# Optimization experiments

Hardware: AMD Instinct MI355X
Metric: run time of the kernel (lower is better)

Reference implementation:

```python
import jax, jax.numpy as jnp
import numpy as np

N_EMBED = 1024
HEAD_COUNT = 16
HEAD_SIZE = 64  # HEAD_COUNT * HEAD_SIZE == N_EMBED
SEQ = 2048
BATCH = 2


def setup_inputs() -> dict:
    key = jax.random.key(0)
    k_ix, k_q, k_k, k_v, k_p, k_b = jax.random.split(key, 6)
    scale = 1.0 / np.sqrt(N_EMBED)
    inp = {
        "ix": jax.random.normal(k_ix, (BATCH, SEQ, N_EMBED), dtype=jnp.float32),
        # per-head projection weights, stored as x @ W form: [H, C, D]
        "Wq": jax.random.normal(k_q, (HEAD_COUNT, N_EMBED, HEAD_SIZE), dtype=jnp.float32) * scale,
        "Wk": jax.random.normal(k_k, (HEAD_COUNT, N_EMBED, HEAD_SIZE), dtype=jnp.float32) * scale,
        "Wv": jax.random.normal(k_v, (HEAD_COUNT, N_EMBED, HEAD_SIZE), dtype=jnp.float32) * scale,
        # output projection (Linear with bias): y = x @ Wp + bp
        "Wp": jax.random.normal(k_p, (N_EMBED, N_EMBED), dtype=jnp.float32) * scale,
        "bp": jax.random.normal(k_b, (N_EMBED,), dtype=jnp.float32) * scale,
    }
    return inp


def reference(ix, Wq, Wk, Wv, Wp, bp):
    B, T, C = ix.shape
    # per-head projections: [B, H, T, D]
    Q = jnp.einsum("btc,hcd->bhtd", ix, Wq)
    K = jnp.einsum("btc,hcd->bhtd", ix, Wk)
    V = jnp.einsum("btc,hcd->bhtd", ix, Wv)
    # NOTE: faithful to source -- scores are MULTIPLIED by sqrt(C) (C = n_embed)
    scores = jnp.einsum("bhtd,bhsd->bhts", Q, K) * (C ** 0.5)
    causal = jnp.tril(jnp.ones((T, T), dtype=bool))
    scores = jnp.where(causal, scores, -jnp.inf)
    wei = jax.nn.softmax(scores, axis=-1)
    out = jnp.einsum("bhts,bhsd->bhtd", wei, V)
    # concat heads (matches torch.cat over per-head outputs along last dim)
    out = out.transpose(0, 2, 1, 3).reshape(B, T, -1)
    return out @ Wp + bp
```

## Files before the change

kernel.cpp:

```cpp
#include <hip/hip_runtime.h>

#define BATCH 2
#define SEQL  2048
#define NEMB  1024
#define NH    16
#define HD    64
#define MROWS (BATCH*SEQL)

typedef short bf16x8 __attribute__((ext_vector_type(8)));
typedef float f32x16 __attribute__((ext_vector_type(16)));

__device__ __forceinline__ unsigned short f2bf(float x) {
    union { float f; unsigned u; } v; v.f = x;
    unsigned r = v.u + 0x7FFFu + ((v.u >> 16) & 1u);
    return (unsigned short)(r >> 16);
}
__device__ __forceinline__ void split_bf16(float x, unsigned short& hi, unsigned short& lo) {
    hi = f2bf(x);
    union { unsigned u; float f; } h; h.u = ((unsigned)hi) << 16;
    lo = f2bf(x - h.f);
}

__device__ __forceinline__ int slot16(int chunk, int lane) {
    return chunk * 66 + (lane & 31) + 33 * (lane >> 5);
}

__global__ __launch_bounds__(256) void split_convert_kernel(
    const float* __restrict__ src,
    unsigned short* __restrict__ dhi, unsigned short* __restrict__ dlo)
{
    int i = (blockIdx.x * 256 + threadIdx.x) * 4;
    float4 v = *(const float4*)(src + i);
    unsigned short h[4], l[4];
    split_bf16(v.x, h[0], l[0]); split_bf16(v.y, h[1], l[1]);
    split_bf16(v.z, h[2], l[2]); split_bf16(v.w, h[3], l[3]);
    uint2 ph, pl;
    ph.x = h[0] | ((unsigned)h[1] << 16); ph.y = h[2] | ((unsigned)h[3] << 16);
    pl.x = l[0] | ((unsigned)l[1] << 16); pl.y = l[2] | ((unsigned)l[3] << 16);
    *(uint2*)(dhi + i) = ph;
    *(uint2*)(dlo + i) = pl;
}

__global__ __launch_bounds__(256) void transpose_convert_kernel(
    const float* __restrict__ Wq, const float* __restrict__ Wk,
    const float* __restrict__ Wv, const float* __restrict__ Wp,
    unsigned short* __restrict__ qhi, unsigned short* __restrict__ qlo,
    unsigned short* __restrict__ khi, unsigned short* __restrict__ klo,
    unsigned short* __restrict__ vhi, unsigned short* __restrict__ pt)
{
    __shared__ float tile[64][68];
    const int z = blockIdx.z, hb = blockIdx.y, c0 = blockIdx.x * 64;
    const float* src; int rstride; unsigned short* dhi; unsigned short* dlo;
    if (z == 0)      { src = Wq + (size_t)hb * 65536; rstride = 64;   dhi = qhi; dlo = qlo; }
    else if (z == 1) { src = Wk + (size_t)hb * 65536; rstride = 64;   dhi = khi; dlo = klo; }
    else if (z == 2) { src = Wv + (size_t)hb * 65536; rstride = 64;   dhi = vhi; dlo = nullptr; }
    else             { src = Wp + (size_t)hb * 64;    rstride = 1024; dhi = pt;  dlo = nullptr; }
    const int tid = threadIdx.x;
    #pragma unroll
    for (int i = 0; i < 4; ++i) {
        int fidx = i * 256 + tid;
        int r  = fidx >> 4;
        int dq = (fidx & 15) * 4;
        float4 v = *(const float4*)(src + (size_t)(c0 + r) * rstride + dq);
        *(float4*)&tile[r][dq] = v;
    }
    __syncthreads();
    #pragma unroll
    for (int i = 0; i < 4; ++i) {
        int fidx = i * 256 + tid;
        int d  = fidx >> 4;
        int cq = (fidx & 15) * 4;
        size_t base = (size_t)(hb * 64 + d) * 1024 + c0 + cq;
        unsigned short hh[4], ll[4];
        #pragma unroll
        for (int j = 0; j < 4; ++j) split_bf16(tile[cq + j][d], hh[j], ll[j]);
        uint2 ph; ph.x = hh[0] | ((unsigned)hh[1] << 16); ph.y = hh[2] | ((unsigned)hh[3] << 16);
        *(uint2*)(dhi + base) = ph;
        if (dlo) {
            uint2 pl; pl.x = ll[0] | ((unsigned)ll[1] << 16); pl.y = ll[2] | ((unsigned)ll[3] << 16);
            *(uint2*)(dlo + base) = pl;
        }
    }
}

__global__ __launch_bounds__(256, 2) void qkv_gemm(
    const unsigned short* __restrict__ Ahi, const unsigned short* __restrict__ Alo,
    const unsigned short* __restrict__ Bq_hi, const unsigned short* __restrict__ Bq_lo,
    const unsigned short* __restrict__ Bk_hi, const unsigned short* __restrict__ Bk_lo,
    const unsigned short* __restrict__ Bv_hi,
    unsigned short* __restrict__ Qhi, unsigned short* __restrict__ Qlo,
    unsigned short* __restrict__ Khi, unsigned short* __restrict__ Klo,
    unsigned short* __restrict__ Vt)
{
    __shared__ unsigned short smem[2][4][4224];

    const int z = blockIdx.z;
    const bool split = (z < 2);
    const unsigned short* __restrict__ Bhi = (z == 0) ? Bq_hi : (z == 1) ? Bk_hi : Bv_hi;
    const unsigned short* __restrict__ Blo = (z == 0) ? Bq_lo : Bk_lo;
    unsigned short* __restrict__ Ohi = (z == 0) ? Qhi : Khi;
    unsigned short* __restrict__ Olo = (z == 0) ? Qlo : Klo;
    const float oscale = (z == 0) ? 32.0f : 1.0f;

    const int m0 = blockIdx.x * 128;
    const int n0 = blockIdx.y * 128;
    const int tid  = threadIdx.x;
    const int wid  = tid >> 6, lane = tid & 63;
    const int wr   = wid >> 1, wc = wid & 1;

    int roff_[2], slot_[2];
    #pragma unroll
    for (int q = 0; q < 2; ++q) {
        int f   = q * 256 + tid;
        int row = f >> 2;
        int k8  = (f & 3) * 8;
        roff_[q] = row * 1024 + k8;
        slot_[q] = slot16((row >> 5) * 2 + (k8 >> 4), (row & 31) + 32 * ((k8 >> 3) & 1)) * 8;
    }
    const unsigned short* __restrict__ Ah = Ahi + (size_t)m0 * 1024;
    const unsigned short* __restrict__ Bh = Bhi + (size_t)n0 * 1024;
    const unsigned short* __restrict__ Al = split ? Alo + (size_t)m0 * 1024 : Ahi;
    const unsigned short* __restrict__ Bl = split ? Blo + (size_t)n0 * 1024 : Bhi;

    bf16x8 pah[2], pbh[2], pal[2], pbl[2];

    #define LOADT(KK)  do { _Pragma("unroll")                                   \
        for (int q = 0; q < 2; ++q) {                                           \
            pah[q] = *(const bf16x8*)(Ah + roff_[q] + (KK));                    \
            pbh[q] = *(const bf16x8*)(Bh + roff_[q] + (KK));                    \
            if (split) {                                                        \
                pal[q] = *(const bf16x8*)(Al + roff_[q] + (KK));                \
                pbl[q] = *(const bf16x8*)(Bl + roff_[q] + (KK));                \
            }                                                                   \
        } } while (0)

    #define WRITET(NB) do { _Pragma("unroll")                                   \
        for (int q = 0; q < 2; ++q) {                                           \
            *(bf16x8*)(&smem[NB][0][slot_[q]]) = pah[q];                        \
            *(bf16x8*)(&smem[NB][1][slot_[q]]) = pbh[q];                        \
            if (split) {                                                        \
                *(bf16x8*)(&smem[NB][2][slot_[q]]) = pal[q];                    \
                *(bf16x8*)(&smem[NB][3][slot_[q]]) = pbl[q];                    \
            }                                                                   \
        } } while (0)

    f32x16 acc[2][2] = {};

    LOADT(0);
    WRITET(0);
    LOADT(32);

    for (int t = 0; t < 32; ++t) {
        __syncthreads();
        if (t + 1 < 32) {
            WRITET((t + 1) & 1);
            if (t + 2 < 32) LOADT((t + 2) * 32);
        }
        const int cb = t & 1;
        const unsigned short* a_hi = smem[cb][0];
        const unsigned short* b_hi = smem[cb][1];
        const unsigned short* a_lo = smem[cb][2];
        const unsigned short* b_lo = smem[cb][3];

        #pragma unroll
        for (int kch = 0; kch < 2; ++kch) {
            bf16x8 ah[2], bh_[2];
            #pragma unroll
            for (int mt = 0; mt < 2; ++mt)
                ah[mt] = *(const bf16x8*)(a_hi + slot16((2 * wr + mt) * 2 + kch, lane) * 8);
            #pragma unroll
            for (int nt = 0; nt < 2; ++nt)
                bh_[nt] = *(const bf16x8*)(b_hi + slot16((2 * wc + nt) * 2 + kch, lane) * 8);
            if (split) {
                bf16x8 al[2], bl[2];
                #pragma unroll
                for (int mt = 0; mt < 2; ++mt)
                    al[mt] = *(const bf16x8*)(a_lo + slot16((2 * wr + mt) * 2 + kch, lane) * 8);
                #pragma unroll
                for (int nt = 0; nt < 2; ++nt)
                    bl[nt] = *(const bf16x8*)(b_lo + slot16((2 * wc + nt) * 2 + kch, lane) * 8);
                #pragma unroll
                for (int mt = 0; mt < 2; ++mt)
                    #pragma unroll
                    for (int nt = 0; nt < 2; ++nt) {
                        acc[mt][nt] = __builtin_amdgcn_mfma_f32_32x32x16_bf16(ah[mt], bh_[nt], acc[mt][nt], 0, 0, 0);
                        acc[mt][nt] = __builtin_amdgcn_mfma_f32_32x32x16_bf16(ah[mt], bl[nt],  acc[mt][nt], 0, 0, 0);
                        acc[mt][nt] = __builtin_amdgcn_mfma_f32_32x32x16_bf16(al[mt], bh_[nt], acc[mt][nt], 0, 0, 0);
                    }
            } else {
                #pragma unroll
                for (int mt = 0; mt < 2; ++mt)
                    #pragma unroll
                    for (int nt = 0; nt < 2; ++nt)
                        acc[mt][nt] = __builtin_amdgcn_mfma_f32_32x32x16_bf16(bh_[nt], ah[mt], acc[mt][nt], 0, 0, 0);
            }
        }
    }
    #undef LOADT
    #undef WRITET

    #pragma unroll
    for (int mt = 0; mt < 2; ++mt) {
        #pragma unroll
        for (int nt = 0; nt < 2; ++nt) {
            if (z == 2) {
                const int mcol = m0 + wr * 64 + mt * 32 + (lane & 31);
                const int bb = mcol >> 11, tt = mcol & (SEQL - 1);
                #pragma unroll
                for (int r = 0; r < 16; ++r) {
                    int nrow = n0 + wc * 64 + nt * 32 + (r & 3) + 8 * (r >> 2) + 4 * (lane >> 5);
                    int head = nrow >> 6, dd = nrow & 63;
                    Vt[((size_t)(bb * NH + head) * HD + dd) * SEQL + tt] = f2bf(acc[mt][nt][r]);
                }
            } else {
                const int ncol = n0 + wc * 64 + nt * 32 + (lane & 31);
                const int head = ncol >> 6, d = ncol & 63;
                #pragma unroll
                for (int r = 0; r < 16; ++r) {
                    int mrow = m0 + wr * 64 + mt * 32 + (r & 3) + 8 * (r >> 2) + 4 * (lane >> 5);
                    int bb = mrow >> 11, t = mrow & (SEQL - 1);
                    size_t idx = ((size_t)(bb * NH + head) * SEQL + t) * HD + d;
                    float v = acc[mt][nt][r] * oscale;
                    unsigned short hi = f2bf(v);
                    Ohi[idx] = hi;
                    union { unsigned u; float f; } hf; hf.u = ((unsigned)hi) << 16;
                    Olo[idx] = f2bf(v - hf.f);
                }
            }
        }
    }
}

__global__ __launch_bounds__(256) void attn_mfma_kernel(
    const unsigned short* __restrict__ Qhi, const unsigned short* __restrict__ Qlo,
    const unsigned short* __restrict__ Khi, const unsigned short* __restrict__ Klo,
    const unsigned short* __restrict__ Vt,
    unsigned short* __restrict__ AO)
{
    __shared__ unsigned short smem[2][3][4224];

    const int bid = blockIdx.x;
    const int xcd = bid & 7;
    const int idx = bid >> 3;
    const int bh  = xcd * 4 + (idx & 3);
    const int g   = 15 - (idx >> 2);

    const int tid  = threadIdx.x;
    const int wid  = tid >> 6;
    const int lane = tid & 63;
    const int ln   = lane & 31;
    const int h    = lane >> 5;

    const int qb_idx = g * 4 + wid;
    const int qb     = qb_idx * 32;
    const int qglob  = qb + ln;
    const int my_nt  = (qb_idx >> 1) + 1;
    const int tmax   = 2 * g + 2;

    const unsigned short* __restrict__ Qbh = Qhi + (size_t)bh * SEQL * HD;
    const unsigned short* __restrict__ Qbl = Qlo + (size_t)bh * SEQL * HD;
    const unsigned short* __restrict__ Kbh = Khi + (size_t)bh * SEQL * HD;
    const unsigned short* __restrict__ Kbl = Klo + (size_t)bh * SEQL * HD;
    const unsigned short* __restrict__ Vtb = Vt  + (size_t)bh * HD * SEQL;

    bf16x8 qhi[4], qlo[4];
    #pragma unroll
    for (int c = 0; c < 4; ++c) {
        qhi[c] = *(const bf16x8*)(Qbh + (size_t)qglob * HD + c * 16 + h * 8);
        qlo[c] = *(const bf16x8*)(Qbl + (size_t)qglob * HD + c * 16 + h * 8);
    }

    int s_[2], d8_[2], ks_[2];
    #pragma unroll
    for (int ff = 0; ff < 2; ++ff) {
        int fidx = ff * 256 + tid;
        s_[ff]  = fidx >> 3;
        d8_[ff] = fidx & 7;
        ks_[ff] = slot16((s_[ff] >> 5) * 4 + (d8_[ff] >> 1),
                         (s_[ff] & 31) + 32 * (d8_[ff] & 1)) * 8;
    }

    bf16x8 kh[2], kl[2], vv[2];
    #pragma unroll
    for (int ff = 0; ff < 2; ++ff) {
        kh[ff] = *(const bf16x8*)(Kbh + (size_t)s_[ff] * HD + d8_[ff] * 8);
        kl[ff] = *(const bf16x8*)(Kbl + (size_t)s_[ff] * HD + d8_[ff] * 8);
        vv[ff] = *(const bf16x8*)(Vtb + (size_t)s_[ff] * SEQL + d8_[ff] * 8);
    }
    #pragma unroll
    for (int ff = 0; ff < 2; ++ff) {
        *(bf16x8*)(&smem[0][0][ks_[ff]]) = kh[ff];
        *(bf16x8*)(&smem[0][1][ks_[ff]]) = kl[ff];
        *(bf16x8*)(&smem[0][2][ks_[ff]]) = vv[ff];
    }
    if (tmax > 1) {
        #pragma unroll
        for (int ff = 0; ff < 2; ++ff) {
            kh[ff] = *(const bf16x8*)(Kbh + (size_t)(64 + s_[ff]) * HD + d8_[ff] * 8);
            kl[ff] = *(const bf16x8*)(Kbl + (size_t)(64 + s_[ff]) * HD + d8_[ff] * 8);
            vv[ff] = *(const bf16x8*)(Vtb + (size_t)s_[ff] * SEQL + 64 + d8_[ff] * 8);
        }
    }

    f32x16 oacc[2] = {};
    float m_run = -1e30f, l_run = 0.f;

    for (int t = 0; t < tmax; ++t) {
        __syncthreads();
        if (t + 1 < tmax) {
            const int nb = (t + 1) & 1;
            #pragma unroll
            for (int ff = 0; ff < 2; ++ff) {
                *(bf16x8*)(&smem[nb][0][ks_[ff]]) = kh[ff];
                *(bf16x8*)(&smem[nb][1][ks_[ff]]) = kl[ff];
                *(bf16x8*)(&smem[nb][2][ks_[ff]]) = vv[ff];
            }
            if (t + 2 < tmax) {
                const int s0n = (t + 2) * 64;
                #pragma unroll
                for (int ff = 0; ff < 2; ++ff) {
                    kh[ff] = *(const bf16x8*)(Kbh + (size_t)(s0n + s_[ff]) * HD + d8_[ff] * 8);
                    kl[ff] = *(const bf16x8*)(Kbl + (size_t)(s0n + s_[ff]) * HD + d8_[ff] * 8);
                    vv[ff] = *(const bf16x8*)(Vtb + (size_t)s_[ff] * SEQL + s0n + d8_[ff] * 8);
                }
            }
        }

        if (t < my_nt) {
            const int cb = t & 1;
            const int s0 = t * 64;
            const bf16x8* khf = (const bf16x8*)&smem[cb][0][0];
            const bf16x8* klf = (const bf16x8*)&smem[cb][1][0];
            const bf16x8* vtf = (const bf16x8*)&smem[cb][2][0];

            f32x16 sacc[2] = {};
            __builtin_amdgcn_s_setprio(1);
            #pragma unroll
            for (int sb = 0; sb < 2; ++sb) {
                #pragma unroll
                for (int c = 0; c < 4; ++c) {
                    bf16x8 ah = khf[slot16(sb * 4 + c, lane)];
                    bf16x8 al = klf[slot16(sb * 4 + c, lane)];
                    sacc[sb] = __builtin_amdgcn_mfma_f32_32x32x16_bf16(ah, qhi[c], sacc[sb], 0, 0, 0);
                    sacc[sb] = __builtin_amdgcn_mfma_f32_32x32x16_bf16(ah, qlo[c], sacc[sb], 0, 0, 0);
                    sacc[sb] = __builtin_amdgcn_mfma_f32_32x32x16_bf16(al, qhi[c], sacc[sb], 0, 0, 0);
                }
            }
            __builtin_amdgcn_s_setprio(0);

            const bool diag = (s0 + 63) > qb;
            float mtile = -1e30f;
            #pragma unroll
            for (int sb = 0; sb < 2; ++sb) {
                #pragma unroll
                for (int r = 0; r < 16; ++r) {
                    int srow = (r & 3) + 8 * (r >> 2) + 4 * h + sb * 32;
                    float x = sacc[sb][r];
                    if (diag && (s0 + srow) > qglob) x = -1e30f;
                    sacc[sb][r] = x;
                    mtile = fmaxf(mtile, x);
                }
            }
            mtile = fmaxf(mtile, __shfl_xor(mtile, 32));
            const float mnew  = fmaxf(m_run, mtile);
            const float alpha = __expf(m_run - mnew);

            float psum = 0.f;
            unsigned pw[2][8];
            #pragma unroll
            for (int sb = 0; sb < 2; ++sb) {
                #pragma unroll
                for (int r2 = 0; r2 < 8; ++r2) {
                    float p0 = __expf(sacc[sb][2 * r2]     - mnew);
                    float p1 = __expf(sacc[sb][2 * r2 + 1] - mnew);
                    psum += p0 + p1;
                    pw[sb][r2] = (unsigned)f2bf(p0) | ((unsigned)f2bf(p1) << 16);
                }
            }
            psum += __shfl_xor(psum, 32);
            l_run = l_run * alpha + psum;
            m_run = mnew;
            #pragma unroll
            for (int dt = 0; dt < 2; ++dt)
                #pragma unroll
                for (int r = 0; r < 16; ++r)
                    oacc[dt][r] *= alpha;

            unsigned px[2][8];
            #pragma unroll
            for (int sb = 0; sb < 2; ++sb)
                #pragma unroll
                for (int i = 0; i < 8; ++i)
                    px[sb][i] = __shfl_xor(pw[sb][i], 32);

            bf16x8 pfrag[4];
            #pragma unroll
            for (int sb = 0; sb < 2; ++sb) {
                #pragma unroll
                for (int c = 0; c < 2; ++c) {
                    unsigned u0, u1, u2, u3;
                    if (h == 0) { u0 = pw[sb][4*c];   u1 = pw[sb][4*c+1]; u2 = px[sb][4*c];   u3 = px[sb][4*c+1]; }
                    else        { u0 = px[sb][4*c+2]; u1 = px[sb][4*c+3]; u2 = pw[sb][4*c+2]; u3 = pw[sb][4*c+3]; }
                    union { unsigned u[4]; bf16x8 v; } cvt;
                    cvt.u[0] = u0; cvt.u[1] = u1; cvt.u[2] = u2; cvt.u[3] = u3;
                    pfrag[sb * 2 + c] = cvt.v;
                }
            }

            __builtin_amdgcn_s_setprio(1);
            #pragma unroll
            for (int dt = 0; dt < 2; ++dt)
                #pragma unroll
                for (int sc = 0; sc < 4; ++sc)
                    oacc[dt] = __builtin_amdgcn_mfma_f32_32x32x16_bf16(
                        vtf[slot16(dt * 4 + sc, lane)], pfrag[sc], oacc[dt], 0, 0, 0);
            __builtin_amdgcn_s_setprio(0);
        }
    }

    const float inv = 1.0f / l_run;
    unsigned short* aop = AO + ((size_t)(bh >> 4) * SEQL + qglob) * NEMB + (bh & 15) * HD;
    #pragma unroll
    for (int dt = 0; dt < 2; ++dt) {
        #pragma unroll
        for (int rg = 0; rg < 4; ++rg) {
            int d0 = dt * 32 + rg * 8 + h * 4;
            unsigned short b0 = f2bf(oacc[dt][rg * 4 + 0] * inv);
            unsigned short b1 = f2bf(oacc[dt][rg * 4 + 1] * inv);
            unsigned short b2 = f2bf(oacc[dt][rg * 4 + 2] * inv);
            unsigned short b3 = f2bf(oacc[dt][rg * 4 + 3] * inv);
            uint2 w;
            w.x = (unsigned)b0 | ((unsigned)b1 << 16);
            w.y = (unsigned)b2 | ((unsigned)b3 << 16);
            *(uint2*)(aop + d0) = w;
        }
    }
}

__global__ __launch_bounds__(256, 2) void out_proj_kernel(
    const unsigned short* __restrict__ A, const unsigned short* __restrict__ B,
    const float* __restrict__ bias, float* __restrict__ out)
{
    __shared__ unsigned short smem[2][2][4224];

    const int m0 = blockIdx.x * 128;
    const int n0 = blockIdx.y * 128;
    const int tid  = threadIdx.x;
    const int wid  = tid >> 6, lane = tid & 63;
    const int wr   = wid >> 1, wc = wid & 1;

    int roff_[2], slot_[2];
    #pragma unroll
    for (int q = 0; q < 2; ++q) {
        int f   = q * 256 + tid;
        int row = f >> 2;
        int k8  = (f & 3) * 8;
        roff_[q] = row * 1024 + k8;
        slot_[q] = slot16((row >> 5) * 2 + (k8 >> 4), (row & 31) + 32 * ((k8 >> 3) & 1)) * 8;
    }
    const unsigned short* __restrict__ Ab = A + (size_t)m0 * 1024;
    const unsigned short* __restrict__ Bb = B + (size_t)n0 * 1024;

    bf16x8 pa[2], pb[2];
    #pragma unroll
    for (int q = 0; q < 2; ++q) {
        pa[q] = *(const bf16x8*)(Ab + roff_[q]);
        pb[q] = *(const bf16x8*)(Bb + roff_[q]);
    }
    #pragma unroll
    for (int q = 0; q < 2; ++q) {
        *(bf16x8*)(&smem[0][0][slot_[q]]) = pa[q];
        *(bf16x8*)(&smem[0][1][slot_[q]]) = pb[q];
    }
    #pragma unroll
    for (int q = 0; q < 2; ++q) {
        pa[q] = *(const bf16x8*)(Ab + roff_[q] + 32);
        pb[q] = *(const bf16x8*)(Bb + roff_[q] + 32);
    }

    f32x16 acc[2][2] = {};

    for (int t = 0; t < 32; ++t) {
        __syncthreads();
        if (t + 1 < 32) {
            const int nb = (t + 1) & 1;
            #pragma unroll
            for (int q = 0; q < 2; ++q) {
                *(bf16x8*)(&smem[nb][0][slot_[q]]) = pa[q];
                *(bf16x8*)(&smem[nb][1][slot_[q]]) = pb[q];
            }
            if (t + 2 < 32) {
                #pragma unroll
                for (int q = 0; q < 2; ++q) {
                    pa[q] = *(const bf16x8*)(Ab + roff_[q] + (t + 2) * 32);
                    pb[q] = *(const bf16x8*)(Bb + roff_[q] + (t + 2) * 32);
                }
            }
        }
        const int cb = t & 1;
        const unsigned short* a_s = smem[cb][0];
        const unsigned short* b_s = smem[cb][1];
        #pragma unroll
        for (int kch = 0; kch < 2; ++kch) {
            bf16x8 ah[2], bh_[2];
            #pragma unroll
            for (int mt = 0; mt < 2; ++mt)
                ah[mt] = *(const bf16x8*)(a_s + slot16((2 * wr + mt) * 2 + kch, lane) * 8);
            #pragma unroll
            for (int nt = 0; nt < 2; ++nt)
                bh_[nt] = *(const bf16x8*)(b_s + slot16((2 * wc + nt) * 2 + kch, lane) * 8);
            #pragma unroll
            for (int mt = 0; mt < 2; ++mt)
                #pragma unroll
                for (int nt = 0; nt < 2; ++nt)
                    acc[mt][nt] = __builtin_amdgcn_mfma_f32_32x32x16_bf16(ah[mt], bh_[nt], acc[mt][nt], 0, 0, 0);
        }
    }

    #pragma unroll
    for (int mt = 0; mt < 2; ++mt) {
        #pragma unroll
        for (int nt = 0; nt < 2; ++nt) {
            const int ncol = n0 + wc * 64 + nt * 32 + (lane & 31);
            const float bv = bias[ncol];
            #pragma unroll
            for (int r = 0; r < 16; ++r) {
                int mrow = m0 + wr * 64 + mt * 32 + (r & 3) + 8 * (r >> 2) + 4 * (lane >> 5);
                out[(size_t)mrow * 1024 + ncol] = acc[mt][nt][r] + bv;
            }
        }
    }
}

extern "C" void kernel_launch(void* const* d_in, const int* in_sizes, int n_in,
                              void* d_out, int out_size, void* d_ws, size_t ws_size,
                              hipStream_t stream)
{
    const float* ix = (const float*)d_in[0];
    const float* Wq = (const float*)d_in[1];
    const float* Wk = (const float*)d_in[2];
    const float* Wv = (const float*)d_in[3];
    const float* Wp = (const float*)d_in[4];
    const float* bp = (const float*)d_in[5];
    float* out = (float*)d_out;

    char* ws = (char*)d_ws;
    #define WSOFF(mb) ((unsigned short*)(ws + (size_t)(mb) * 1024 * 1024))
    unsigned short* ix_hi  = WSOFF(0);
    unsigned short* ix_lo  = WSOFF(8);
    unsigned short* Wqt_hi = WSOFF(16);
    unsigned short* Wqt_lo = WSOFF(18);
    unsigned short* Wkt_hi = WSOFF(20);
    unsigned short* Wkt_lo = WSOFF(22);
    unsigned short* Wvt_hi = WSOFF(24);
    unsigned short* Qhi    = WSOFF(26);
    unsigned short* Qlo    = WSOFF(34);
    unsigned short* Khi    = WSOFF(42);
    unsigned short* Klo    = WSOFF(50);
    unsigned short* Wpt    = WSOFF(58);
    unsigned short* AObf   = WSOFF(0);
    unsigned short* Vt     = (unsigned short*)d_out;
    #undef WSOFF

    split_convert_kernel<<<MROWS * NEMB / 4 / 256, 256, 0, stream>>>(ix, ix_hi, ix_lo);
    transpose_convert_kernel<<<dim3(16, 16, 4), 256, 0, stream>>>(
        Wq, Wk, Wv, Wp, Wqt_hi, Wqt_lo, Wkt_hi, Wkt_lo, Wvt_hi, Wpt);
    qkv_gemm<<<dim3(MROWS / 128, NEMB / 128, 3), 256, 0, stream>>>(
        ix_hi, ix_lo, Wqt_hi, Wqt_lo, Wkt_hi, Wkt_lo, Wvt_hi,
        Qhi, Qlo, Khi, Klo, Vt);
    attn_mfma_kernel<<<512, 256, 0, stream>>>(Qhi, Qlo, Khi, Klo, Vt, AObf);
    out_proj_kernel<<<dim3(MROWS / 128, NEMB / 128), 256, 0, stream>>>(AObf, Wpt, bp, out);
}
```

Measured before the change: 193.4 us.

## Load V directly into registers, skip softmax rescales, use hardware bf16 packing

V fragments are now read straight from global memory into registers for each tile instead of being staged through double-buffered shared memory, which shrinks LDS use and removes one set of shared stores and loads. Q is prescaled by sqrt(C)*log2(e) so the softmax can use exp2. The running max is only updated, and the accumulators only rescaled, when a tile's max exceeds it by more than a threshold, which skips most rescale work. bf16 packing switches to v_cvt_pk_bf16_f32, and the cross-half shuffles become v_permlane32_swap. The risks are exposed global-load latency for V and possible overflow or precision drift from the lazy rescale threshold.

New measurement: 214.5 us. 10.9% more time.

```diff
diff --git a/kernel.cpp b/kernel.cpp
--- a/kernel.cpp
+++ b/kernel.cpp
@@ -7,6 +7,8 @@
 #define HD    64
 #define MROWS (BATCH*SEQL)
 
+#define QSCALE 46.166241308446828f
+
 typedef short bf16x8 __attribute__((ext_vector_type(8)));
 typedef float f32x16 __attribute__((ext_vector_type(16)));
 
@@ -19,6 +21,14 @@
     hi = f2bf(x);
     union { unsigned u; float f; } h; h.u = ((unsigned)hi) << 16;
     lo = f2bf(x - h.f);
+}
+__device__ __forceinline__ unsigned cvt_pk_bf16(float a, float b) {
+    unsigned r;
+    asm("v_cvt_pk_bf16_f32 %0, %1, %2" : "=v"(r) : "v"(a), "v"(b));
+    return r;
+}
+__device__ __forceinline__ void plane_swap(unsigned& a, unsigned& b) {
+    asm volatile("v_permlane32_swap_b32 %0, %1" : "+v"(a), "+v"(b));
 }
 
 __device__ __forceinline__ int slot16(int chunk, int lane) {
@@ -100,7 +110,7 @@
     const unsigned short* __restrict__ Blo = (z == 0) ? Bq_lo : Bk_lo;
     unsigned short* __restrict__ Ohi = (z == 0) ? Qhi : Khi;
     unsigned short* __restrict__ Olo = (z == 0) ? Qlo : Klo;
-    const float oscale = (z == 0) ? 32.0f : 1.0f;
+    const float oscale = (z == 0) ? QSCALE : 1.0f;
 
     const int m0 = blockIdx.x * 128;
     const int n0 = blockIdx.y * 128;
@@ -237,7 +247,7 @@
     const unsigned short* __restrict__ Vt,
     unsigned short* __restrict__ AO)
 {
-    __shared__ unsigned short smem[2][3][4224];
+    __shared__ unsigned short smem[2][2][4224];
 
     const int bid = blockIdx.x;
     const int xcd = bid & 7;
@@ -279,26 +289,24 @@
         ks_[ff] = slot16((s_[ff] >> 5) * 4 + (d8_[ff] >> 1),
                          (s_[ff] & 31) + 32 * (d8_[ff] & 1)) * 8;
     }
-
-    bf16x8 kh[2], kl[2], vv[2];
+    const size_t voff = (size_t)ln * SEQL + h * 8;
+
+    bf16x8 kh[2], kl[2];
     #pragma unroll
     for (int ff = 0; ff < 2; ++ff) {
         kh[ff] = *(const bf16x8*)(Kbh + (size_t)s_[ff] * HD + d8_[ff] * 8);
         kl[ff] = *(const bf16x8*)(Kbl + (size_t)s_[ff] * HD + d8_[ff] * 8);
-        vv[ff] = *(const bf16x8*)(Vtb + (size_t)s_[ff] * SEQL + d8_[ff] * 8);
     }
     #pragma unroll
     for (int ff = 0; ff < 2; ++ff) {
         *(bf16x8*)(&smem[0][0][ks_[ff]]) = kh[ff];
         *(bf16x8*)(&smem[0][1][ks_[ff]]) = kl[ff];
-        *(bf16x8*)(&smem[0][2][ks_[ff]]) = vv[ff];
     }
     if (tmax > 1) {
         #pragma unroll
         for (int ff = 0; ff < 2; ++ff) {
             kh[ff] = *(const bf16x8*)(Kbh + (size_t)(64 + s_[ff]) * HD + d8_[ff] * 8);
             kl[ff] = *(const bf16x8*)(Kbl + (size_t)(64 + s_[ff]) * HD + d8_[ff] * 8);
-            vv[ff] = *(const bf16x8*)(Vtb + (size_t)s_[ff] * SEQL + 64 + d8_[ff] * 8);
         }
     }
 
@@ -307,13 +315,24 @@
 
     for (int t = 0; t < tmax; ++t) {
         __syncthreads();
+        const int s0 = t * 64;
+
+        bf16x8 vf[8];
+        if (t < my_nt) {
+            #pragma unroll
+            for (int dt = 0; dt < 2; ++dt)
+                #pragma unroll
+                for (int sc = 0; sc < 4; ++sc)
+                    vf[dt * 4 + sc] = *(const bf16x8*)(
+                        Vtb + (size_t)dt * 32 * SEQL + voff + s0 + sc * 16);
+        }
+
         if (t + 1 < tmax) {
             const int nb = (t + 1) & 1;
             #pragma unroll
             for (int ff = 0; ff < 2; ++ff) {
                 *(bf16x8*)(&smem[nb][0][ks_[ff]]) = kh[ff];
                 *(bf16x8*)(&smem[nb][1][ks_[ff]]) = kl[ff];
-                *(bf16x8*)(&smem[nb][2][ks_[ff]]) = vv[ff];
             }
             if (t + 2 < tmax) {
                 const int s0n = (t + 2) * 64;
@@ -321,17 +340,14 @@
                 for (int ff = 0; ff < 2; ++ff) {
                     kh[ff] = *(const bf16x8*)(Kbh + (size_t)(s0n + s_[ff]) * HD + d8_[ff] * 8);
                     kl[ff] = *(const bf16x8*)(Kbl + (size_t)(s0n + s_[ff]) * HD + d8_[ff] * 8);
-                    vv[ff] = *(const bf16x8*)(Vtb + (size_t)s_[ff] * SEQL + s0n + d8_[ff] * 8);
                 }
             }
         }
 
         if (t < my_nt) {
             const int cb = t & 1;
-            const int s0 = t * 64;
             const bf16x8* khf = (const bf16x8*)&smem[cb][0][0];
             const bf16x8* klf = (const bf16x8*)&smem[cb][1][0];
-            const bf16x8* vtf = (const bf16x8*)&smem[cb][2][0];
 
             f32x16 sacc[2] = {};
             __builtin_amdgcn_s_setprio(1);
@@ -362,8 +378,18 @@
                 }
             }
             mtile = fmaxf(mtile, __shfl_xor(mtile, 32));
-            const float mnew  = fmaxf(m_run, mtile);
-            const float alpha = __expf(m_run - mnew);
+
+            if (!__all(mtile - m_run <= 11.5f)) {
+                const float mnew  = fmaxf(m_run, mtile);
+                const float alpha = exp2f(m_run - mnew);
+                l_run *= alpha;
+                #pragma unroll
+                for (int dt = 0; dt < 2; ++dt)
+                    #pragma unroll
+                    for (int r = 0; r < 16; ++r)
+                        oacc[dt][r] *= alpha;
+                m_run = mnew;
+            }
 
             float psum = 0.f;
             unsigned pw[2][8];
@@ -371,36 +397,24 @@
             for (int sb = 0; sb < 2; ++sb) {
                 #pragma unroll
                 for (int r2 = 0; r2 < 8; ++r2) {
-                    float p0 = __expf(sacc[sb][2 * r2]     - mnew);
-                    float p1 = __expf(sacc[sb][2 * r2 + 1] - mnew);
+                    float p0 = exp2f(sacc[sb][2 * r2]     - m_run);
+                    float p1 = exp2f(sacc[sb][2 * r2 + 1] - m_run);
                     psum += p0 + p1;
-                    pw[sb][r2] = (unsigned)f2bf(p0) | ((unsigned)f2bf(p1) << 16);
+                    pw[sb][r2] = cvt_pk_bf16(p0, p1);
                 }
             }
             psum += __shfl_xor(psum, 32);
-            l_run = l_run * alpha + psum;
-            m_run = mnew;
-            #pragma unroll
-            for (int dt = 0; dt < 2; ++dt)
-                #pragma unroll
-                for (int r = 0; r < 16; ++r)
-                    oacc[dt][r] *= alpha;
-
-            unsigned px[2][8];
-            #pragma unroll
-            for (int sb = 0; sb < 2; ++sb)
-                #pragma unroll
-                for (int i = 0; i < 8; ++i)
-                    px[sb][i] = __shfl_xor(pw[sb][i], 32);
+            l_run += psum;
 
             bf16x8 pfrag[4];
             #pragma unroll
             for (int sb = 0; sb < 2; ++sb) {
                 #pragma unroll
                 for (int c = 0; c < 2; ++c) {
-                    unsigned u0, u1, u2, u3;
-                    if (h == 0) { u0 = pw[sb][4*c];   u1 = pw[sb][4*c+1]; u2 = px[sb][4*c];   u3 = px[sb][4*c+1]; }
-                    else        { u0 = px[sb][4*c+2]; u1 = px[sb][4*c+3]; u2 = pw[sb][4*c+2]; u3 = pw[sb][4*c+3]; }
+                    unsigned u0 = pw[sb][4 * c + 0], u2 = pw[sb][4 * c + 2];
+                    unsigned u1 = pw[sb][4 * c + 1], u3 = pw[sb][4 * c + 3];
+                    plane_swap(u0, u2);
+                    plane_swap(u1, u3);
                     union { unsigned u[4]; bf16x8 v; } cvt;
                     cvt.u[0] = u0; cvt.u[1] = u1; cvt.u[2] = u2; cvt.u[3] = u3;
                     pfrag[sb * 2 + c] = cvt.v;
@@ -413,7 +427,7 @@
                 #pragma unroll
                 for (int sc = 0; sc < 4; ++sc)
                     oacc[dt] = __builtin_amdgcn_mfma_f32_32x32x16_bf16(
-                        vtf[slot16(dt * 4 + sc, lane)], pfrag[sc], oacc[dt], 0, 0, 0);
+                        vf[dt * 4 + sc], pfrag[sc], oacc[dt], 0, 0, 0);
             __builtin_amdgcn_s_setprio(0);
         }
     }
@@ -425,13 +439,9 @@
         #pragma unroll
         for (int rg = 0; rg < 4; ++rg) {
             int d0 = dt * 32 + rg * 8 + h * 4;
-            unsigned short b0 = f2bf(oacc[dt][rg * 4 + 0] * inv);
-            unsigned short b1 = f2bf(oacc[dt][rg * 4 + 1] * inv);
-            unsigned short b2 = f2bf(oacc[dt][rg * 4 + 2] * inv);
-            unsigned short b3 = f2bf(oacc[dt][rg * 4 + 3] * inv);
             uint2 w;
-            w.x = (unsigned)b0 | ((unsigned)b1 << 16);
-            w.y = (unsigned)b2 | ((unsigned)b3 << 16);
+            w.x = cvt_pk_bf16(oacc[dt][rg * 4 + 0] * inv, oacc[dt][rg * 4 + 1] * inv);
+            w.y = cvt_pk_bf16(oacc[dt][rg * 4 + 2] * inv, oacc[dt][rg * 4 + 3] * inv);
             *(uint2*)(aop + d0) = w;
         }
     }
```
